# Kernel optimization log

Measured on AMD Instinct MI355X. Metric: run time of the kernel, lower is better.

Reference implementation:

```python
import jax, jax.numpy as jnp
import numpy as np

# CRPConfig defaults
KAPPA = 1.0
C = 0.95
ALPHA = 0.05
EPS = 1e-8
T_MAX = 32
MARGIN_FACTOR = 2.0

B, I, HD, L = 512, 1024, 2048, 1000


def setup_inputs() -> dict:
    key = jax.random.key(0)
    k0, k1, k2, k3 = jax.random.split(key, 4)
    x = jax.random.normal(k0, (B, I), jnp.float32)
    # kaiming-like scaling keeps activations numerically sane
    RIH = jax.random.normal(k1, (I, HD), jnp.float32) * np.float32(1.0 / np.sqrt(I))
    RH = jax.random.normal(k2, (HD, HD), jnp.float32) * np.float32(1.0 / np.sqrt(HD))
    RHL = jax.random.normal(k3, (HD, L), jnp.float32) * np.float32(1.0 / np.sqrt(HD))
    BH = jnp.zeros((HD,), jnp.float32)
    BL = jnp.zeros((L,), jnp.float32)
    MIH = jnp.ones((I, HD), jnp.float32)
    MH = jnp.ones((HD, HD), jnp.float32)
    MHL = jnp.ones((HD, L), jnp.float32)
    return {"x": x, "RIH": RIH, "RH": RH, "RHL": RHL, "BH": BH, "BL": BL,
            "MIH": MIH, "MH": MH, "MHL": MHL}


def _crp_forward(x, RIH, RH, RHL, BH, BL, MIH, MH, MHL):
    # build weights
    W_IH = RIH * MIH                      # [I, H]
    W_HL = RHL * MHL                      # [H, L]
    RHm = RH * MH                         # [H, H]
    # normalize so max column L1 <= c (value only; straight-through grad)
    col_l1 = jnp.abs(RHm).sum(axis=0)
    scale = C / jnp.maximum(col_l1.max(), EPS)
    W_H = jax.lax.stop_gradient(RHm * scale) + RHm - jax.lax.stop_gradient(RHm)

    rho = 1.0 - KAPPA + KAPPA * C
    denom = max(1e-12, 1.0 - rho)
    whl_inf = jnp.abs(W_HL).sum(axis=0).max()
    gamma_coef = whl_inf * (rho / denom)

    drive = x @ W_IH + BH                 # constant across steps, [B, H]
    Bsz = x.shape[0]
    Hs0 = jnp.zeros((Bsz, HD), x.dtype)
    active0 = jnp.ones((Bsz,), jnp.bool_)
    tau0 = jnp.full((Bsz,), T_MAX, jnp.int32)
    cert0 = jnp.zeros((Bsz,), jnp.bool_)
    logits_tau0 = jnp.zeros((Bsz, L), x.dtype)

    def step(carry, t):
        Hs, active, tau, certified, logits_tau = carry
        pre = Hs @ W_H + drive
        act = jnp.where(pre >= 0, pre, ALPHA * pre)      # LeakyReLU
        H_cand = (1.0 - KAPPA) * Hs + KAPPA * act
        H_next = jnp.where(active[:, None], H_cand, Hs)
        logits = H_next @ W_HL + BL
        # certification
        dH = jnp.max(jnp.abs(H_next - Hs), axis=1)       # H_prev == Hs
        Gamma = gamma_coef * dH
        top2 = jax.lax.top_k(logits, 2)[0]
        margin = top2[:, 0] - top2[:, 1]
        newly = active & (margin > MARGIN_FACTOR * Gamma)
        tau = jnp.where(newly, t, tau)
        certified = certified | newly
        logits_tau = jnp.where(newly[:, None], logits, logits_tau)
        active = active & (~newly)
        return (H_next, active, tau, certified, logits_tau), None

    ts = jnp.arange(1, T_MAX + 1, dtype=jnp.int32)
    (Hf, active, tau, certified, logits_tau), _ = jax.lax.scan(
        step, (Hs0, active0, tau0, cert0, logits_tau0), ts)

    never = ~certified
    logits_last = Hf @ W_HL + BL
    logits_tau = jnp.where(never[:, None], logits_last, logits_tau)
    return logits_tau


def reference(x, RIH, RH, RHL, BH, BL, MIH, MH, MHL):
    return _crp_forward(x, RIH, RH, RHL, BH, BL, MIH, MH, MHL)
```

## Files before the change

### kernel.cpp

```cpp
#include <hip/hip_runtime.h>

typedef __attribute__((ext_vector_type(8))) short short8;
typedef __attribute__((ext_vector_type(4))) float f32x4;

static constexpr int BN    = 512;
static constexpr int ID    = 1024;
static constexpr int HDm   = 2048;
static constexpr int LD    = 1000;
static constexpr int TMAXc = 32;
static constexpr float ALPHAc = 0.05f;

__device__ __forceinline__ unsigned short f2bf(float x) {
    unsigned u = __float_as_uint(x);
    u += 0x7fffu + ((u >> 16) & 1u);
    return (unsigned short)(u >> 16);
}
__device__ __forceinline__ float bf2f(unsigned short h) {
    return __uint_as_float(((unsigned)h) << 16);
}
__device__ __forceinline__ void split2(float x, unsigned short& hi, unsigned short& lo) {
    hi = f2bf(x);
    lo = f2bf(x - bf2f(hi));
}

__device__ __forceinline__ void gload16(const void* g, void* l) {
    __builtin_amdgcn_global_load_lds(
        (const __attribute__((address_space(1))) unsigned int*)g,
        (__attribute__((address_space(3))) unsigned int*)l, 16, 0, 0);
}


__device__ __forceinline__ size_t himg_off(int gr, int gc) {
    const int rt = gr >> 6, ar = gr & 63, kc = gc >> 7, ac = gc & 127;
    const int byte = (ar * 256 + ac * 2) ^ ((ar & 15) << 4);
    return ((size_t)(rt * 16 + kc) << 14) + byte;
}

__device__ __forceinline__ void tile64_drive(
    const float* __restrict__ Af, int lda, int row0,
    const unsigned short* __restrict__ BThi, const unsigned short* __restrict__ BTlo,
    int ldk, int col0, int K, char* lds, f32x4& acc, int& s_out, int& p_out)
{
    char* Ah = lds;
    char* Al = lds + 16384;
    char* Bh = lds + 32768;
    char* Bl = lds + 40960;
    const int t = threadIdx.x, lane = t & 63, w = t >> 6;
    const int s = w & 7, p = w >> 3;
    s_out = s; p_out = p;
    f32x4 z = {0.f, 0.f, 0.f, 0.f};
    acc = z;

    const int ar = t >> 4, ac = (t & 15) << 3;
    const int br = t >> 5, bc = (t & 31) << 2;
    const int asb = (ar * 256 + ac * 2) ^ ((ar & 15) << 4);
    const int bsb = (br * 256 + bc * 2) ^ ((br & 15) << 4);
    const float* Ap = Af + (size_t)(row0 + ar) * lda + ac;
    const unsigned short* Bhp = BThi + (size_t)(col0 + br) * ldk + bc;
    const unsigned short* Blp = BTlo + (size_t)(col0 + br) * ldk + bc;

    const int frow = s >> 1, fcol = s & 1;
    const int arow = frow * 16 + (lane & 15);
    const int colr = fcol * 16 + (lane & 15);
    const int ab0 = arow * 256, bb0 = colr * 256;
    const int axor = (arow & 15) << 4, bxor = (colr & 15) << 4;
    const int kwin = p * 128 + ((lane >> 4) << 4);

    float4 af0a = *(const float4*)(Ap),       af0b = *(const float4*)(Ap + 4);
    float4 af1a = *(const float4*)(Ap + 128), af1b = *(const float4*)(Ap + 132);
    uint2 bh0 = *(const uint2*)(Bhp),       bl0 = *(const uint2*)(Blp);
    uint2 bh1 = *(const uint2*)(Bhp + 128), bl1 = *(const uint2*)(Blp + 128);

    for (int k0 = 0; k0 < K; k0 += 128) {
        unsigned short h[8], l[8];
        const float vv[8] = {af0a.x, af0a.y, af0a.z, af0a.w,
                             af0b.x, af0b.y, af0b.z, af0b.w};
#pragma unroll
        for (int i = 0; i < 8; ++i) split2(vv[i], h[i], l[i]);
        uint4 awh = make_uint4((unsigned)h[0] | ((unsigned)h[1] << 16),
                               (unsigned)h[2] | ((unsigned)h[3] << 16),
                               (unsigned)h[4] | ((unsigned)h[5] << 16),
                               (unsigned)h[6] | ((unsigned)h[7] << 16));
        uint4 awl = make_uint4((unsigned)l[0] | ((unsigned)l[1] << 16),
                               (unsigned)l[2] | ((unsigned)l[3] << 16),
                               (unsigned)l[4] | ((unsigned)l[5] << 16),
                               (unsigned)l[6] | ((unsigned)l[7] << 16));
        const uint2 bwh = bh0, bwl = bl0;
        __syncthreads();
        *(uint4*)(Ah + asb) = awh;
        *(uint4*)(Al + asb) = awl;
        *(uint2*)(Bh + bsb) = bwh;
        *(uint2*)(Bl + bsb) = bwl;
        af0a = af1a; af0b = af1b;
        bh0 = bh1; bl0 = bl1;
        if (k0 + 256 < K) {
            af1a = *(const float4*)(Ap + k0 + 256);
            af1b = *(const float4*)(Ap + k0 + 260);
            bh1 = *(const uint2*)(Bhp + k0 + 256);
            bl1 = *(const uint2*)(Blp + k0 + 256);
        }
        __syncthreads();
#pragma unroll
        for (int ks = 0; ks < 2; ++ks) {
            const int kb = kwin + ks * 64;
            short8 bh = *(const short8*)(Bh + ((bb0 + kb) ^ bxor));
            short8 bl = *(const short8*)(Bl + ((bb0 + kb) ^ bxor));
            short8 ah = *(const short8*)(Ah + ((ab0 + kb) ^ axor));
            short8 al = *(const short8*)(Al + ((ab0 + kb) ^ axor));
            acc = __builtin_amdgcn_mfma_f32_16x16x32_bf16(ah, bh, acc, 0, 0, 0);
            acc = __builtin_amdgcn_mfma_f32_16x16x32_bf16(al, bh, acc, 0, 0, 0);
            acc = __builtin_amdgcn_mfma_f32_16x16x32_bf16(ah, bl, acc, 0, 0, 0);
        }
    }
}

__device__ __forceinline__ void tile64_img(
    const char* __restrict__ Ahi, const char* __restrict__ Alo,
    const char* __restrict__ Bhi, const char* __restrict__ Blo,
    char* lds, f32x4& acc, int& s_out, int& p_out)
{
    char* Ah = lds;
    char* Al = lds + 16384;
    char* Bh = lds + 32768;
    char* Bl = lds + 40960;
    const int t = threadIdx.x, lane = t & 63, w = t >> 6;
    const int s = w & 7, p = w >> 3;
    s_out = s; p_out = p;
    f32x4 z = {0.f, 0.f, 0.f, 0.f};
    acc = z;

    const int frow = s >> 1, fcol = s & 1;
    const int arow = frow * 16 + (lane & 15);
    const int colr = fcol * 16 + (lane & 15);
    const int ab0 = arow * 256, bb0 = colr * 256;
    const int axor = (arow & 15) << 4, bxor = (colr & 15) << 4;
    const int kwin = p * 128 + ((lane >> 4) << 4);
    const int t16 = t * 16;

    for (int kc = 0; kc < 16; ++kc) {
        __syncthreads();
        gload16(Ahi + ((size_t)kc << 14) + t16, Ah + (w << 10));
        gload16(Alo + ((size_t)kc << 14) + t16, Al + (w << 10));
        if (w < 8) gload16(Bhi + ((size_t)kc << 13) + t16, Bh + (w << 10));
        else       gload16(Blo + ((size_t)kc << 13) + t16 - 8192, Bl + ((w - 8) << 10));
        __syncthreads();
#pragma unroll
        for (int ks = 0; ks < 2; ++ks) {
            const int kb = kwin + ks * 64;
            short8 bh = *(const short8*)(Bh + ((bb0 + kb) ^ bxor));
            short8 bl = *(const short8*)(Bl + ((bb0 + kb) ^ bxor));
            short8 ah = *(const short8*)(Ah + ((ab0 + kb) ^ axor));
            short8 al = *(const short8*)(Al + ((ab0 + kb) ^ axor));
            acc = __builtin_amdgcn_mfma_f32_16x16x32_bf16(ah, bh, acc, 0, 0, 0);
            acc = __builtin_amdgcn_mfma_f32_16x16x32_bf16(al, bh, acc, 0, 0, 0);
            acc = __builtin_amdgcn_mfma_f32_16x16x32_bf16(ah, bl, acc, 0, 0, 0);
        }
    }
}

__device__ __forceinline__ void tile32_img(
    const char* __restrict__ Ahi, const char* __restrict__ Alo,
    const char* __restrict__ Bhi, const char* __restrict__ Blo,
    char* lds, f32x4& acc, int& s_out, int& p_out)
{
    char* Ah = lds;
    char* Al = lds + 8192;
    char* Bh = lds + 16384;
    char* Bl = lds + 24576;
    const int t = threadIdx.x, lane = t & 63, w = t >> 6;
    const int s = w & 3, p = w >> 2;
    s_out = s; p_out = p;
    f32x4 z = {0.f, 0.f, 0.f, 0.f};
    acc = z;

    const int frow = s >> 1, fcol = s & 1;
    const int arow = frow * 16 + (lane & 15);
    const int colr = fcol * 16 + (lane & 15);
    const int ab0 = arow * 256, bb0 = colr * 256;
    const int axor = (arow & 15) << 4, bxor = (colr & 15) << 4;
    const int kwin = p * 64 + ((lane >> 4) << 4);
    const int t16 = t * 16;

    for (int kc = 0; kc < 16; ++kc) {
        __syncthreads();
        if (w < 8) {
            gload16(Ahi + ((size_t)kc << 14) + t16, Ah + (w << 10));
            gload16(Bhi + ((size_t)kc << 13) + t16, Bh + (w << 10));
        } else {
            gload16(Alo + ((size_t)kc << 14) + t16 - 8192, Al + ((w - 8) << 10));
            gload16(Blo + ((size_t)kc << 13) + t16 - 8192, Bl + ((w - 8) << 10));
        }
        __syncthreads();
        const int kb = kwin;
        short8 bh = *(const short8*)(Bh + ((bb0 + kb) ^ bxor));
        short8 bl = *(const short8*)(Bl + ((bb0 + kb) ^ bxor));
        short8 ah = *(const short8*)(Ah + ((ab0 + kb) ^ axor));
        short8 al = *(const short8*)(Al + ((ab0 + kb) ^ axor));
        acc = __builtin_amdgcn_mfma_f32_16x16x32_bf16(ah, bh, acc, 0, 0, 0);
        acc = __builtin_amdgcn_mfma_f32_16x16x32_bf16(al, bh, acc, 0, 0, 0);
        acc = __builtin_amdgcn_mfma_f32_16x16x32_bf16(ah, bl, acc, 0, 0, 0);
    }
}

__global__ void k_init(int* active, int* cnt, float* scal,
                       float* margS, float* drift, int* fresh)
{
    int i = blockIdx.x * blockDim.x + threadIdx.x;
    if (i < 2 * BN) {
        active[i] = 1;
        margS[i] = 3.4e38f;
        drift[i] = 0.f;
        fresh[i] = 1;
    }
    if (i < 16) cnt[i] = 64;
    if (i < 8) scal[i] = 0.f;
}

__global__ __launch_bounds__(256) void k_colsum_wh(const float* __restrict__ RH,
                                                   const float* __restrict__ MH,
                                                   float* __restrict__ part)
{
    const int colTile = blockIdx.x >> 3, rs = blockIdx.x & 7;
    const int col = colTile * 64 + (threadIdx.x & 63);
    const int rq = threadIdx.x >> 6;
    const int r0 = rs * 256;
    float s = 0.f;
    for (int i = r0 + rq; i < r0 + 256; i += 4)
        s += fabsf(RH[(size_t)i * HDm + col] * MH[(size_t)i * HDm + col]);
    __shared__ float red[4][64];
    red[rq][threadIdx.x & 63] = s;
    __syncthreads();
    if (threadIdx.x < 64)
        part[(size_t)rs * HDm + col] = red[0][threadIdx.x] + red[1][threadIdx.x] +
                                       red[2][threadIdx.x] + red[3][threadIdx.x];
}

__global__ __launch_bounds__(256) void k_colsum_whl(const float* __restrict__ RHL,
                                                    const float* __restrict__ MHL,
                                                    float* __restrict__ part)
{
    const int colTile = blockIdx.x >> 3, rs = blockIdx.x & 7;
    const int col = colTile * 64 + (threadIdx.x & 63);
    const int rq = threadIdx.x >> 6;
    const int r0 = rs * 256;
    float s = 0.f;
    if (col < LD) {
        for (int i = r0 + rq; i < r0 + 256; i += 4)
            s += fabsf(RHL[(size_t)i * LD + col] * MHL[(size_t)i * LD + col]);
    }
    __shared__ float red[4][64];
    red[rq][threadIdx.x & 63] = s;
    __syncthreads();
    if (threadIdx.x < 64)
        part[(size_t)rs * 1024 + col] = red[0][threadIdx.x] + red[1][threadIdx.x] +
                                        red[2][threadIdx.x] + red[3][threadIdx.x];
}

__global__ __launch_bounds__(1024) void k_scalars(const float* __restrict__ part_wh,
                                                  const float* __restrict__ part_whl,
                                                  float* scal)
{
    float m1 = 0.f, m2 = 0.f;
    for (int c = threadIdx.x; c < HDm; c += 1024) {
        float s = 0.f;
#pragma unroll
        for (int k = 0; k < 8; ++k) s += part_wh[(size_t)k * HDm + c];
        m1 = fmaxf(m1, s);
    }
    {
        const int c = threadIdx.x;
        if (c < 1024) {
            float s = 0.f;
#pragma unroll
            for (int k = 0; k < 8; ++k) s += part_whl[(size_t)k * 1024 + c];
            m2 = fmaxf(m2, s);
        }
    }
#pragma unroll
    for (int off = 1; off < 64; off <<= 1) {
        m1 = fmaxf(m1, __shfl_xor(m1, off));
        m2 = fmaxf(m2, __shfl_xor(m2, off));
    }
    __shared__ float r1[16], r2[16];
    if ((threadIdx.x & 63) == 0) { r1[threadIdx.x >> 6] = m1; r2[threadIdx.x >> 6] = m2; }
    __syncthreads();
    if (threadIdx.x == 0) {
        float a = 0.f, b = 0.f;
#pragma unroll
        for (int i = 0; i < 16; ++i) { a = fmaxf(a, r1[i]); b = fmaxf(b, r2[i]); }
        scal[2] = 0.95f / fmaxf(a, 1e-8f);
        scal[3] = b * 19.f;
    }
}

__global__ __launch_bounds__(256) void k_wsplit(
    const float* __restrict__ R, const float* __restrict__ M,
    unsigned short* __restrict__ Ohi, unsigned short* __restrict__ Olo,
    int NR, int NC, int NCp, const float* __restrict__ scal, int scidx)
{
    __shared__ float T[64][65];
    const int nct = NCp >> 6;
    const int c0 = (blockIdx.x % nct) << 6;
    const int r0 = (blockIdx.x / nct) << 6;
    const float s = (scidx >= 0) ? scal[scidx] : 1.f;
    const int t = threadIdx.x;
    const int ir = t >> 2, ics = (t & 3) << 4;
#pragma unroll
    for (int i = 0; i < 16; ++i) {
        const int c = c0 + ics + i;
        float v = 0.f;
        if (c < NC) {
            const size_t idx = (size_t)(r0 + ir) * NC + c;
            v = R[idx] * M[idx] * s;
        }
        T[ir][ics + i] = v;
    }
    __syncthreads();
    const int oc = t >> 2, ors = (t & 3) << 4;
    unsigned short hb[16], lb[16];
#pragma unroll
    for (int i = 0; i < 16; ++i) split2(T[ors + i][oc], hb[i], lb[i]);
    const size_t base = (size_t)(c0 + oc) * NR + r0 + ors;
    uint4 v;
    v.x = hb[0] | ((unsigned)hb[1] << 16);  v.y = hb[2] | ((unsigned)hb[3] << 16);
    v.z = hb[4] | ((unsigned)hb[5] << 16);  v.w = hb[6] | ((unsigned)hb[7] << 16);
    *(uint4*)(Ohi + base) = v;
    v.x = hb[8] | ((unsigned)hb[9] << 16);  v.y = hb[10] | ((unsigned)hb[11] << 16);
    v.z = hb[12] | ((unsigned)hb[13] << 16); v.w = hb[14] | ((unsigned)hb[15] << 16);
    *(uint4*)(Ohi + base + 8) = v;
    v.x = lb[0] | ((unsigned)lb[1] << 16);  v.y = lb[2] | ((unsigned)lb[3] << 16);
    v.z = lb[4] | ((unsigned)lb[5] << 16);  v.w = lb[6] | ((unsigned)lb[7] << 16);
    *(uint4*)(Olo + base) = v;
    v.x = lb[8] | ((unsigned)lb[9] << 16);  v.y = lb[10] | ((unsigned)lb[11] << 16);
    v.z = lb[12] | ((unsigned)lb[13] << 16); v.w = lb[14] | ((unsigned)lb[15] << 16);
    *(uint4*)(Olo + base + 8) = v;
}

__global__ __launch_bounds__(256) void k_wsplit_img(
    const float* __restrict__ R, const float* __restrict__ M,
    char* __restrict__ imghi, char* __restrict__ imglo,
    int NC, int nkc, const float* __restrict__ scal, int scidx)
{
    const int ct = blockIdx.x / nkc, kc = blockIdx.x % nkc;
    const float s = (scidx >= 0) ? scal[scidx] : 1.f;
    char* hi = imghi + ((size_t)(ct * nkc + kc) << 13);
    char* lo = imglo + ((size_t)(ct * nkc + kc) << 13);
#pragma unroll
    for (int i = 0; i < 16; ++i) {
        const int idx = i * 256 + threadIdx.x;
        const int br = idx & 31, bc = idx >> 5;
        const int c = ct * 32 + br;
        const int k = kc * 128 + bc;
        float v = 0.f;
        if (c < NC) { const size_t a = (size_t)k * NC + c; v = R[a] * M[a] * s; }
        unsigned short h, l;
        split2(v, h, l);
        const int byte = (br * 256 + bc * 2) ^ ((br & 15) << 4);
        *(unsigned short*)(hi + byte) = h;
        *(unsigned short*)(lo + byte) = l;
    }
}

__global__ __launch_bounds__(1024, 8) void k_drive_mfma(
    const float* __restrict__ x,
    const unsigned short* __restrict__ WIHThi, const unsigned short* __restrict__ WIHTlo,
    const float* __restrict__ BH, float* __restrict__ drive)
{
    __shared__ char lds[49152];
    f32x4 acc;
    int s, p;
    const int row0 = (blockIdx.x >> 6) * 64, col0 = (blockIdx.x & 63) * 32;
    tile64_drive(x, ID, row0, WIHThi, WIHTlo, ID, col0, ID, lds, acc, s, p);
    const int lane = threadIdx.x & 63;
    __syncthreads();
    f32x4* red = (f32x4*)lds;
    if (p == 1) red[s * 64 + lane] = acc;
    __syncthreads();
    if (p == 0) {
        f32x4 o = red[s * 64 + lane];
        acc += o;
        const int frow = s >> 1, fcol = s & 1;
        const int gc = col0 + fcol * 16 + (lane & 15);
        const int gr0 = row0 + frow * 16 + ((lane >> 4) << 2);
        const float bh = BH[gc];
#pragma unroll
        for (int r = 0; r < 4; ++r)
            drive[(size_t)(gr0 + r) * HDm + gc] = acc[r] + bh;
    }
}

__global__ __launch_bounds__(1024, 8) void k_p1(
    const char* __restrict__ WHhi, const char* __restrict__ WHlo,
    const float* __restrict__ drive,
    char* __restrict__ HAhi, char* __restrict__ HAlo,
    char* __restrict__ HBhi, char* __restrict__ HBlo,
    const float* __restrict__ logits, float* __restrict__ out,
    int* __restrict__ active, int* __restrict__ cnt, const float* __restrict__ scal,
    float* __restrict__ dhp, const float* __restrict__ m1p, const float* __restrict__ m2p,
    float* __restrict__ margS, float* __restrict__ drift, const int* __restrict__ fresh,
    int t)
{
    __shared__ char lds[49152];
    __shared__ int sact[64], snew[64];
    __shared__ int s_cnt;
    const int pp = (t - 1) & 1, pc = t & 1;
    {
        const int* cp = cnt + pp * 8;
        int sum = 0;
#pragma unroll
        for (int i = 0; i < 8; ++i) sum += cp[i];
        if (sum == 0) return;
    }
    const int bid = blockIdx.x, tid = threadIdx.x;
    const int rt = bid >> 6, row0m = rt << 6, col0 = (bid & 63) * 32;
    const int* actP = active + pp * BN;
    int* actC = active + pc * BN;
    const char* Hshi = (t & 1) ? HAhi : HBhi;
    const char* Hslo = (t & 1) ? HAlo : HBlo;
    char* Hnhi = (t & 1) ? HBhi : HAhi;
    char* Hnlo = (t & 1) ? HBlo : HAlo;
    const float* dhpP = dhp + (size_t)pp * BN * 64;
    float* dhpC = dhp + (size_t)pc * BN * 64;
    const float* margSP = margS + pp * BN;
    float* margSC = margS + pc * BN;
    const float* driftP = drift + pp * BN;
    float* driftC = drift + pc * BN;
    const int* freshP = fresh + pp * BN;

    if (t > 1) {
        const float gamma2 = 2.f * scal[3];
        const int rl = tid >> 4, j = tid & 15;
        const int r = row0m + rl;
        const int act = actP[r];
        const int fr = freshP[r];
        float dh = fmaxf(fmaxf(dhpP[(size_t)r * 64 + j],      dhpP[(size_t)r * 64 + 16 + j]),
                         fmaxf(dhpP[(size_t)r * 64 + 32 + j], dhpP[(size_t)r * 64 + 48 + j]));
        float M1 = m1p[(size_t)r * 32 + j], M2 = m2p[(size_t)r * 32 + j];
        {
            float o1 = m1p[(size_t)r * 32 + 16 + j], o2 = m2p[(size_t)r * 32 + 16 + j];
            if (o1 > M1) { M2 = fmaxf(M1, o2); M1 = o1; }
            else M2 = fmaxf(M2, o1);
        }
#pragma unroll
        for (int off = 1; off < 16; off <<= 1) {
            dh = fmaxf(dh, __shfl_xor(dh, off));
            float o1 = __shfl_xor(M1, off), o2 = __shfl_xor(M2, off);
            if (o1 > M1) { M2 = fmaxf(M1, o2); M1 = o1; }
            else M2 = fmaxf(M2, o1);
        }
        if (j == 0) {
            const float marg = M1 - M2;
            int nw = fr && act && (marg > gamma2 * dh);
            snew[rl] = nw;
            sact[rl] = act && !nw;
            margSC[r] = fr ? marg : margSP[r];
            driftC[r] = fr ? 0.f : (driftP[r] + dh);
        }
    } else if (tid < 64) {
        sact[tid] = 1; snew[tid] = 0;
    }
    __syncthreads();
    if (tid < 64) {
        unsigned long long b = __ballot(sact[tid] != 0);
        actC[row0m + tid] = sact[tid];
        if (tid == 0) {
            s_cnt = __popcll(b);
            (cnt + pc * 8)[rt] = s_cnt;
        }
    }
    if (t > 1 && (bid & 63) == 0) {
        for (int rl2 = 0; rl2 < 64; ++rl2) {
            if (snew[rl2]) {
                const float* lr = logits + (size_t)(row0m + rl2) * LD;
                float* orow = out + (size_t)(row0m + rl2) * LD;
                for (int jj = tid; jj < LD; jj += 1024) orow[jj] = lr[jj];
            }
        }
    }
    __syncthreads();
    if (s_cnt == 0) return;

    f32x4 acc;
    int s, p;
    tile64_img(Hshi + ((size_t)(rt * 16) << 14), Hslo + ((size_t)(rt * 16) << 14),
               WHhi + ((size_t)((bid & 63) * 16) << 13), WHlo + ((size_t)((bid & 63) * 16) << 13),
               lds, acc, s, p);
    const int lane = tid & 63;
    __syncthreads();
    f32x4* red = (f32x4*)lds;
    if (p == 1) red[s * 64 + lane] = acc;
    __syncthreads();
    float (*sdh)[2] = (float(*)[2])(lds + 16384);
    if (p == 0) {
        f32x4 o = red[s * 64 + lane];
        acc += o;
        const int frow = s >> 1, fcol = s & 1;
        const int gc = col0 + fcol * 16 + (lane & 15);
        const int gr0 = row0m + frow * 16 + ((lane >> 4) << 2);
        float dh4[4];
#pragma unroll
        for (int r = 0; r < 4; ++r) {
            const int gr = gr0 + r;
            const size_t ia = himg_off(gr, gc);
            const unsigned short oh = *(const unsigned short*)(Hshi + ia);
            const unsigned short ol = *(const unsigned short*)(Hslo + ia);
            const float old = bf2f(oh) + bf2f(ol);
            const int a = sact[gr - row0m];
            unsigned short nh, nl;
            if (a) {
                const float pre = acc[r] + drive[(size_t)gr * HDm + gc];
                const float av = pre >= 0.f ? pre : ALPHAc * pre;
                split2(av, nh, nl);
            } else { nh = oh; nl = ol; }
            *(unsigned short*)(Hnhi + ia) = nh;
            *(unsigned short*)(Hnlo + ia) = nl;
            dh4[r] = fabsf((bf2f(nh) + bf2f(nl)) - old);
        }
#pragma unroll
        for (int off = 1; off < 16; off <<= 1)
#pragma unroll
            for (int r = 0; r < 4; ++r)
                dh4[r] = fmaxf(dh4[r], __shfl_xor(dh4[r], off));
        if ((lane & 15) == 0) {
            const int rl0 = frow * 16 + ((lane >> 4) << 2);
#pragma unroll
            for (int r = 0; r < 4; ++r) sdh[rl0 + r][fcol] = dh4[r];
        }
    }
    __syncthreads();
    if (tid < 64) {
        float d = fmaxf(sdh[tid][0], sdh[tid][1]);
        dhpC[(size_t)(row0m + tid) * 64 + (bid & 63)] = d;
    }
}

__global__ __launch_bounds__(1024, 8) void k_p2(
    const char* __restrict__ WLhi, const char* __restrict__ WLlo,
    const float* __restrict__ BL,
    const char* __restrict__ HAhi, const char* __restrict__ HAlo,
    const char* __restrict__ HBhi, const char* __restrict__ HBlo,
    float* __restrict__ logits, const int* __restrict__ active, const int* __restrict__ cnt,
    float* __restrict__ m1p, float* __restrict__ m2p, const float* __restrict__ scal,
    const float* __restrict__ dhp, const float* __restrict__ margS,
    const float* __restrict__ drift, int* __restrict__ fresh, int t)
{
    __shared__ char lds[33280];
    __shared__ int sposs[32];
    __shared__ int s_go;
    const int pc = t & 1;
    {
        const int* cp = cnt + pc * 8;
        int sum = 0;
#pragma unroll
        for (int i = 0; i < 8; ++i) sum += cp[i];
        if (sum == 0) return;
    }
    const int bid = blockIdx.x, tid = threadIdx.x;
    const char* Hnhi = (t & 1) ? HBhi : HAhi;
    const char* Hnlo = (t & 1) ? HBlo : HAlo;
    const int* actC = active + pc * BN;
    const float* dhpC = dhp + (size_t)pc * BN * 64;
    const float* margSc = margS + pc * BN;
    const float* driftc = drift + pc * BN;
    int* freshC = fresh + pc * BN;
    const int row0 = (bid >> 5) * 32, col0 = (bid & 31) * 32;

    {
        const int rr = tid >> 5, j = tid & 31;
        const int r = row0 + rr;
        float d = fmaxf(dhpC[(size_t)r * 64 + j], dhpC[(size_t)r * 64 + 32 + j]);
#pragma unroll
        for (int off = 1; off < 32; off <<= 1) d = fmaxf(d, __shfl_xor(d, off));
        if (j == 0) {
            const int act = actC[r];
            int poss;
            if (t == TMAXc) poss = act;
            else {
                const float whl = scal[3] * (1.f / 19.f);
                poss = act && (margSc[r] + 2.f * whl * (driftc[r] + d) >
                               0.99f * 38.f * whl * d);
            }
            sposs[rr] = poss;
        }
    }
    __syncthreads();
    if (tid < 64) {
        int v = (tid < 32) ? sposs[tid] : 0;
        unsigned long long b = __ballot(v != 0);
        if (tid == 0) s_go = (b != 0ull);
    }
    __syncthreads();
    if (tid < 32) freshC[row0 + tid] = s_go;
    if (!s_go) return;

    const int rt2 = bid >> 5;
    const char* Ahi = Hnhi + ((size_t)((rt2 >> 1) * 16) << 14) + ((rt2 & 1) << 13);
    const char* Alo = Hnlo + ((size_t)((rt2 >> 1) * 16) << 14) + ((rt2 & 1) << 13);
    f32x4 acc;
    int s, p;
    tile32_img(Ahi, Alo,
               WLhi + ((size_t)((bid & 31) * 16) << 13), WLlo + ((size_t)((bid & 31) * 16) << 13),
               lds, acc, s, p);
    const int lane = tid & 63;
    __syncthreads();
    f32x4* red = (f32x4*)lds;
    if (p > 0) red[(p - 1) * 256 + s * 64 + lane] = acc;
    __syncthreads();
    float (*st1)[2] = (float(*)[2])(lds + 12288);
    float (*st2)[2] = (float(*)[2])(lds + 12544);
    if (p == 0) {
#pragma unroll
        for (int q = 0; q < 3; ++q) {
            f32x4 o = red[q * 256 + s * 64 + lane];
            acc += o;
        }
        const int frow = s >> 1, fcol = s & 1;
        const int gc = col0 + fcol * 16 + (lane & 15);
        const int gr0 = row0 + frow * 16 + ((lane >> 4) << 2);
        const bool okc = gc < LD;
        const float blv = okc ? BL[gc] : 0.f;
        float m1a[4], m2a[4];
#pragma unroll
        for (int r = 0; r < 4; ++r) {
            const float v = acc[r] + blv;
            if (okc) logits[(size_t)(gr0 + r) * LD + gc] = v;
            m1a[r] = okc ? v : -3.4e38f;
            m2a[r] = -3.4e38f;
        }
#pragma unroll
        for (int off = 1; off < 16; off <<= 1) {
#pragma unroll
            for (int r = 0; r < 4; ++r) {
                float o1 = __shfl_xor(m1a[r], off);
                float o2 = __shfl_xor(m2a[r], off);
                if (o1 > m1a[r]) { m2a[r] = fmaxf(m1a[r], o2); m1a[r] = o1; }
                else m2a[r] = fmaxf(m2a[r], o1);
            }
        }
        if ((lane & 15) == 0) {
            const int rl0 = frow * 16 + ((lane >> 4) << 2);
#pragma unroll
            for (int r = 0; r < 4; ++r) {
                st1[rl0 + r][fcol] = m1a[r];
                st2[rl0 + r][fcol] = m2a[r];
            }
        }
    }
    __syncthreads();
    if (tid < 32) {
        float M1 = st1[tid][0], M2 = st2[tid][0];
        {
            float o1 = st1[tid][1], o2 = st2[tid][1];
            if (o1 > M1) { M2 = fmaxf(M1, o2); M1 = o1; }
            else M2 = fmaxf(M2, o1);
        }
        m1p[(size_t)(row0 + tid) * 32 + (bid & 31)] = M1;
        m2p[(size_t)(row0 + tid) * 32 + (bid & 31)] = M2;
    }
}

__global__ __launch_bounds__(1024) void k_tail(
    const float* __restrict__ logits, const int* __restrict__ active,
    float* __restrict__ out)
{
    const int row0 = blockIdx.x * 64;
    for (int rl = 0; rl < 64; ++rl) {
        const int r = row0 + rl;
        if (active[r] && active[BN + r]) {
            const float* lr = logits + (size_t)r * LD;
            float* orow = out + (size_t)r * LD;
            for (int jj = threadIdx.x; jj < LD; jj += 1024) orow[jj] = lr[jj];
        }
    }
}

extern "C" void kernel_launch(void* const* d_in, const int* in_sizes, int n_in,
                              void* d_out, int out_size, void* d_ws, size_t ws_size,
                              hipStream_t stream)
{
    const float* x   = (const float*)d_in[0];
    const float* RIH = (const float*)d_in[1];
    const float* RH  = (const float*)d_in[2];
    const float* RHL = (const float*)d_in[3];
    const float* BH  = (const float*)d_in[4];
    const float* BL  = (const float*)d_in[5];
    const float* MIH = (const float*)d_in[6];
    const float* MH  = (const float*)d_in[7];
    const float* MHL = (const float*)d_in[8];
    float* out = (float*)d_out;
    char* w = (char*)d_ws;

    char* WHhi = w;
    char* WHlo = w + 8388608;
    char* WXhi = w + 16777216;
    char* WXlo = w + 20971520;
    float* drive = (float*)(w + 25165824);
    char* HAhi = w + 29360128;
    char* HAlo = w + 31457280;
    char* HBhi = w + 33554432;
    char* HBlo = w + 35651584;
    float* logits = (float*)(w + 37748736);
    float* scal   = (float*)(w + 39796736);
    int*   active = (int*)(w + 39796800);
    int*   cnt    = (int*)(w + 39800896);
    float* dhp    = (float*)(w + 39800960);
    float* m1p    = (float*)(w + 40063104);
    float* m2p    = (float*)(w + 40128640);
    float* margS  = (float*)(w + 40194176);
    float* drift  = (float*)(w + 40198272);
    int*   fresh  = (int*)(w + 40202368);

    k_init<<<4, 256, 0, stream>>>(active, cnt, scal, margS, drift, fresh);
    k_colsum_wh<<<256, 256, 0, stream>>>(RH, MH, dhp);
    k_colsum_whl<<<128, 256, 0, stream>>>(RHL, MHL, m1p);
    k_scalars<<<1, 1024, 0, stream>>>(dhp, m1p, scal);
    k_wsplit<<<512, 256, 0, stream>>>(RIH, MIH, (unsigned short*)WXhi,
                                      (unsigned short*)WXlo, ID, HDm, HDm, scal, -1);
    k_drive_mfma<<<512, 1024, 0, stream>>>(x, (const unsigned short*)WXhi,
                                           (const unsigned short*)WXlo, BH, drive);
    k_wsplit_img<<<1024, 256, 0, stream>>>(RH, MH, WHhi, WHlo, HDm, 16, scal, 2);
    k_wsplit_img<<<512, 256, 0, stream>>>(RHL, MHL, WXhi, WXlo, LD, 16, scal, -1);
    (void)hipMemsetAsync(HAhi, 0, 4194304, stream);

    for (int t = 1; t <= TMAXc; ++t) {
        k_p1<<<512, 1024, 0, stream>>>(WHhi, WHlo, drive, HAhi, HAlo, HBhi, HBlo,
                                       logits, out, active, cnt, scal, dhp, m1p, m2p,
                                       margS, drift, fresh, t);
        k_p2<<<512, 1024, 0, stream>>>(WXhi, WXlo, BL, HAhi, HAlo, HBhi, HBlo,
                                       logits, active, cnt, m1p, m2p, scal,
                                       dhp, margS, drift, fresh, t);
    }
    k_tail<<<8, 1024, 0, stream>>>(logits, active, out);
}
```

Before: 1.336 ms.

## Double-buffer LDS tiles with 64-wide K chunks in recurrent GEMM kernels

Re-lays out the pre-swizzled weight and hidden-state images into 64-column K chunks instead of 128, and rewrites the per-step tile loops to double-buffer LDS so the next chunk's global-to-LDS load is issued while MFMAs consume the current one. This replaces two block barriers per chunk with a single wait-plus-barrier. The aim is to hide global load latency in the 32-step scan. In the logits kernel, only half the waves now compute and the K-split reduction shrinks from four partial sums to two. The cost is twice as many loop iterations with smaller work per barrier, and idle waves in the second kernel.

New measurement: 1.767 ms. 1.32x slower.

```diff
diff --git a/kernel.cpp b/kernel.cpp
--- a/kernel.cpp
+++ b/kernel.cpp
@@ -31,9 +31,9 @@
 
 
 __device__ __forceinline__ size_t himg_off(int gr, int gc) {
-    const int rt = gr >> 6, ar = gr & 63, kc = gc >> 7, ac = gc & 127;
-    const int byte = (ar * 256 + ac * 2) ^ ((ar & 15) << 4);
-    return ((size_t)(rt * 16 + kc) << 14) + byte;
+    const int rt = gr >> 6, ar = gr & 63, kc = gc >> 6, ac = gc & 63;
+    const int byte = (ar * 128 + ac * 2) ^ ((ar & 15) << 4);
+    return ((size_t)(rt * 32 + kc) << 13) + byte;
 }
 
 __device__ __forceinline__ void tile64_drive(
@@ -114,92 +114,118 @@
     }
 }
 
-__device__ __forceinline__ void tile64_img(
+__device__ __forceinline__ void tile64_pipe(
     const char* __restrict__ Ahi, const char* __restrict__ Alo,
     const char* __restrict__ Bhi, const char* __restrict__ Blo,
     char* lds, f32x4& acc, int& s_out, int& p_out)
 {
-    char* Ah = lds;
-    char* Al = lds + 16384;
-    char* Bh = lds + 32768;
-    char* Bl = lds + 40960;
     const int t = threadIdx.x, lane = t & 63, w = t >> 6;
     const int s = w & 7, p = w >> 3;
     s_out = s; p_out = p;
     f32x4 z = {0.f, 0.f, 0.f, 0.f};
     acc = z;
-
     const int frow = s >> 1, fcol = s & 1;
     const int arow = frow * 16 + (lane & 15);
     const int colr = fcol * 16 + (lane & 15);
-    const int ab0 = arow * 256, bb0 = colr * 256;
     const int axor = (arow & 15) << 4, bxor = (colr & 15) << 4;
-    const int kwin = p * 128 + ((lane >> 4) << 4);
-    const int t16 = t * 16;
-
-    for (int kc = 0; kc < 16; ++kc) {
-        __syncthreads();
-        gload16(Ahi + ((size_t)kc << 14) + t16, Ah + (w << 10));
-        gload16(Alo + ((size_t)kc << 14) + t16, Al + (w << 10));
-        if (w < 8) gload16(Bhi + ((size_t)kc << 13) + t16, Bh + (w << 10));
-        else       gload16(Blo + ((size_t)kc << 13) + t16 - 8192, Bl + ((w - 8) << 10));
-        __syncthreads();
-#pragma unroll
-        for (int ks = 0; ks < 2; ++ks) {
-            const int kb = kwin + ks * 64;
-            short8 bh = *(const short8*)(Bh + ((bb0 + kb) ^ bxor));
-            short8 bl = *(const short8*)(Bl + ((bb0 + kb) ^ bxor));
-            short8 ah = *(const short8*)(Ah + ((ab0 + kb) ^ axor));
-            short8 al = *(const short8*)(Al + ((ab0 + kb) ^ axor));
-            acc = __builtin_amdgcn_mfma_f32_16x16x32_bf16(ah, bh, acc, 0, 0, 0);
-            acc = __builtin_amdgcn_mfma_f32_16x16x32_bf16(al, bh, acc, 0, 0, 0);
-            acc = __builtin_amdgcn_mfma_f32_16x16x32_bf16(ah, bl, acc, 0, 0, 0);
-        }
-    }
-}
-
-__device__ __forceinline__ void tile32_img(
+    const int kwin = p * 64 + ((lane >> 4) << 4);
+    const int abyte = (arow * 128 + kwin) ^ axor;
+    const int bbyte = (colr * 128 + kwin) ^ bxor;
+    const int l16 = lane << 4;
+
+    char* buf0 = lds;
+    char* buf1 = lds + 24576;
+
+#define P1_ISSUE(kc, buf)                                                      \
+    do {                                                                       \
+        if (w < 8) {                                                           \
+            gload16(Ahi + ((size_t)(kc) << 13) + (w << 10) + l16,              \
+                    (buf) + (w << 10));                                        \
+            if (w < 4)                                                         \
+                gload16(Bhi + ((size_t)(kc) << 12) + (w << 10) + l16,          \
+                        (buf) + 16384 + (w << 10));                            \
+            else                                                               \
+                gload16(Blo + ((size_t)(kc) << 12) + ((w - 4) << 10) + l16,    \
+                        (buf) + 20480 + ((w - 4) << 10));                      \
+        } else {                                                               \
+            gload16(Alo + ((size_t)(kc) << 13) + ((w - 8) << 10) + l16,        \
+                    (buf) + 8192 + ((w - 8) << 10));                           \
+        }                                                                      \
+    } while (0)
+
+    P1_ISSUE(0, buf0);
+    for (int kc = 0; kc < 32; ++kc) {
+        char* cur = (kc & 1) ? buf1 : buf0;
+        char* nxt = (kc & 1) ? buf0 : buf1;
+        asm volatile("s_waitcnt vmcnt(0)" ::: "memory");
+        __builtin_amdgcn_sched_barrier(0);
+        __builtin_amdgcn_s_barrier();
+        __builtin_amdgcn_sched_barrier(0);
+        if (kc + 1 < 32) P1_ISSUE(kc + 1, nxt);
+        short8 ah = *(const short8*)(cur + abyte);
+        short8 al = *(const short8*)(cur + 8192 + abyte);
+        short8 bh = *(const short8*)(cur + 16384 + bbyte);
+        short8 bl = *(const short8*)(cur + 20480 + bbyte);
+        acc = __builtin_amdgcn_mfma_f32_16x16x32_bf16(ah, bh, acc, 0, 0, 0);
+        acc = __builtin_amdgcn_mfma_f32_16x16x32_bf16(al, bh, acc, 0, 0, 0);
+        acc = __builtin_amdgcn_mfma_f32_16x16x32_bf16(ah, bl, acc, 0, 0, 0);
+    }
+#undef P1_ISSUE
+}
+
+__device__ __forceinline__ void tile32_pipe(
     const char* __restrict__ Ahi, const char* __restrict__ Alo,
     const char* __restrict__ Bhi, const char* __restrict__ Blo,
     char* lds, f32x4& acc, int& s_out, int& p_out)
 {
-    char* Ah = lds;
-    char* Al = lds + 8192;
-    char* Bh = lds + 16384;
-    char* Bl = lds + 24576;
     const int t = threadIdx.x, lane = t & 63, w = t >> 6;
     const int s = w & 3, p = w >> 2;
     s_out = s; p_out = p;
     f32x4 z = {0.f, 0.f, 0.f, 0.f};
     acc = z;
-
     const int frow = s >> 1, fcol = s & 1;
     const int arow = frow * 16 + (lane & 15);
     const int colr = fcol * 16 + (lane & 15);
-    const int ab0 = arow * 256, bb0 = colr * 256;
     const int axor = (arow & 15) << 4, bxor = (colr & 15) << 4;
-    const int kwin = p * 64 + ((lane >> 4) << 4);
-    const int t16 = t * 16;
-
-    for (int kc = 0; kc < 16; ++kc) {
-        __syncthreads();
-        if (w < 8) {
-            gload16(Ahi + ((size_t)kc << 14) + t16, Ah + (w << 10));
-            gload16(Bhi + ((size_t)kc << 13) + t16, Bh + (w << 10));
-        } else {
-            gload16(Alo + ((size_t)kc << 14) + t16 - 8192, Al + ((w - 8) << 10));
-            gload16(Blo + ((size_t)kc << 13) + t16 - 8192, Bl + ((w - 8) << 10));
-        }
-        __syncthreads();
-        const int kb = kwin;
-        short8 bh = *(const short8*)(Bh + ((bb0 + kb) ^ bxor));
-        short8 bl = *(const short8*)(Bl + ((bb0 + kb) ^ bxor));
-        short8 ah = *(const short8*)(Ah + ((ab0 + kb) ^ axor));
-        short8 al = *(const short8*)(Al + ((ab0 + kb) ^ axor));
-        acc = __builtin_amdgcn_mfma_f32_16x16x32_bf16(ah, bh, acc, 0, 0, 0);
-        acc = __builtin_amdgcn_mfma_f32_16x16x32_bf16(al, bh, acc, 0, 0, 0);
-        acc = __builtin_amdgcn_mfma_f32_16x16x32_bf16(ah, bl, acc, 0, 0, 0);
-    }
+    const int kwin = (p & 1) * 64 + ((lane >> 4) << 4);
+    const int abyte = (arow * 128 + kwin) ^ axor;
+    const int bbyte = (colr * 128 + kwin) ^ bxor;
+    const int g = w & 3;
+    const int l16 = lane << 4;
+
+    char* buf0 = lds;
+    char* buf1 = lds + 16384;
+
+#define P2_ISSUE(kc, buf)                                                      \
+    do {                                                                       \
+        const char* src;                                                       \
+        if (w < 4)       src = Ahi + ((size_t)(kc) << 13) + (g << 10);         \
+        else if (w < 8)  src = Alo + ((size_t)(kc) << 13) + (g << 10);         \
+        else if (w < 12) src = Bhi + ((size_t)(kc) << 12) + (g << 10);         \
+        else             src = Blo + ((size_t)(kc) << 12) + (g << 10);         \
+        gload16(src + l16, (buf) + (w << 10));                                 \
+    } while (0)
+
+    P2_ISSUE(0, buf0);
+    for (int kc = 0; kc < 32; ++kc) {
+        char* cur = (kc & 1) ? buf1 : buf0;
+        char* nxt = (kc & 1) ? buf0 : buf1;
+        asm volatile("s_waitcnt vmcnt(0)" ::: "memory");
+        __builtin_amdgcn_sched_barrier(0);
+        __builtin_amdgcn_s_barrier();
+        __builtin_amdgcn_sched_barrier(0);
+        if (kc + 1 < 32) P2_ISSUE(kc + 1, nxt);
+        if (p < 2) {
+            short8 ah = *(const short8*)(cur + abyte);
+            short8 al = *(const short8*)(cur + 4096 + abyte);
+            short8 bh = *(const short8*)(cur + 8192 + bbyte);
+            short8 bl = *(const short8*)(cur + 12288 + bbyte);
+            acc = __builtin_amdgcn_mfma_f32_16x16x32_bf16(ah, bh, acc, 0, 0, 0);
+            acc = __builtin_amdgcn_mfma_f32_16x16x32_bf16(al, bh, acc, 0, 0, 0);
+            acc = __builtin_amdgcn_mfma_f32_16x16x32_bf16(ah, bl, acc, 0, 0, 0);
+        }
+    }
+#undef P2_ISSUE
 }
 
 __global__ void k_init(int* active, int* cnt, float* scal,
@@ -339,25 +365,24 @@
 __global__ __launch_bounds__(256) void k_wsplit_img(
     const float* __restrict__ R, const float* __restrict__ M,
     char* __restrict__ imghi, char* __restrict__ imglo,
-    int NC, int nkc, const float* __restrict__ scal, int scidx)
-{
-    const int ct = blockIdx.x / nkc, kc = blockIdx.x % nkc;
+    int NC, const float* __restrict__ scal, int scidx)
+{
+    const int ct = blockIdx.x >> 5, kc = blockIdx.x & 31;
     const float s = (scidx >= 0) ? scal[scidx] : 1.f;
-    char* hi = imghi + ((size_t)(ct * nkc + kc) << 13);
-    char* lo = imglo + ((size_t)(ct * nkc + kc) << 13);
-#pragma unroll
-    for (int i = 0; i < 16; ++i) {
+    const size_t base = (size_t)blockIdx.x << 12;
+#pragma unroll
+    for (int i = 0; i < 8; ++i) {
         const int idx = i * 256 + threadIdx.x;
         const int br = idx & 31, bc = idx >> 5;
         const int c = ct * 32 + br;
-        const int k = kc * 128 + bc;
+        const int k = kc * 64 + bc;
         float v = 0.f;
         if (c < NC) { const size_t a = (size_t)k * NC + c; v = R[a] * M[a] * s; }
         unsigned short h, l;
         split2(v, h, l);
-        const int byte = (br * 256 + bc * 2) ^ ((br & 15) << 4);
-        *(unsigned short*)(hi + byte) = h;
-        *(unsigned short*)(lo + byte) = l;
+        const int byte = (br * 128 + bc * 2) ^ ((br & 15) << 4);
+        *(unsigned short*)(imghi + base + byte) = h;
+        *(unsigned short*)(imglo + base + byte) = l;
     }
 }
 
@@ -482,9 +507,9 @@
 
     f32x4 acc;
     int s, p;
-    tile64_img(Hshi + ((size_t)(rt * 16) << 14), Hslo + ((size_t)(rt * 16) << 14),
-               WHhi + ((size_t)((bid & 63) * 16) << 13), WHlo + ((size_t)((bid & 63) * 16) << 13),
-               lds, acc, s, p);
+    tile64_pipe(Hshi + ((size_t)(rt * 32) << 13), Hslo + ((size_t)(rt * 32) << 13),
+                WHhi + ((size_t)((bid & 63) * 32) << 12), WHlo + ((size_t)((bid & 63) * 32) << 12),
+                lds, acc, s, p);
     const int lane = tid & 63;
     __syncthreads();
     f32x4* red = (f32x4*)lds;
@@ -594,26 +619,23 @@
     if (!s_go) return;
 
     const int rt2 = bid >> 5;
-    const char* Ahi = Hnhi + ((size_t)((rt2 >> 1) * 16) << 14) + ((rt2 & 1) << 13);
-    const char* Alo = Hnlo + ((size_t)((rt2 >> 1) * 16) << 14) + ((rt2 & 1) << 13);
+    const char* Ahi = Hnhi + ((size_t)((rt2 >> 1) * 32) << 13) + ((rt2 & 1) << 12);
+    const char* Alo = Hnlo + ((size_t)((rt2 >> 1) * 32) << 13) + ((rt2 & 1) << 12);
     f32x4 acc;
     int s, p;
-    tile32_img(Ahi, Alo,
-               WLhi + ((size_t)((bid & 31) * 16) << 13), WLlo + ((size_t)((bid & 31) * 16) << 13),
-               lds, acc, s, p);
+    tile32_pipe(Ahi, Alo,
+                WLhi + ((size_t)((bid & 31) * 32) << 12), WLlo + ((size_t)((bid & 31) * 32) << 12),
+                lds, acc, s, p);
     const int lane = tid & 63;
     __syncthreads();
     f32x4* red = (f32x4*)lds;
-    if (p > 0) red[(p - 1) * 256 + s * 64 + lane] = acc;
-    __syncthreads();
-    float (*st1)[2] = (float(*)[2])(lds + 12288);
-    float (*st2)[2] = (float(*)[2])(lds + 12544);
+    if (p == 1) red[s * 64 + lane] = acc;
+    __syncthreads();
+    float (*st1)[2] = (float(*)[2])(lds + 8192);
+    float (*st2)[2] = (float(*)[2])(lds + 8448);
     if (p == 0) {
-#pragma unroll
-        for (int q = 0; q < 3; ++q) {
-            f32x4 o = red[q * 256 + s * 64 + lane];
-            acc += o;
-        }
+        f32x4 o = red[s * 64 + lane];
+        acc += o;
         const int frow = s >> 1, fcol = s & 1;
         const int gc = col0 + fcol * 16 + (lane & 15);
         const int gr0 = row0 + frow * 16 + ((lane >> 4) << 2);
@@ -718,8 +740,8 @@
                                       (unsigned short*)WXlo, ID, HDm, HDm, scal, -1);
     k_drive_mfma<<<512, 1024, 0, stream>>>(x, (const unsigned short*)WXhi,
                                            (const unsigned short*)WXlo, BH, drive);
-    k_wsplit_img<<<1024, 256, 0, stream>>>(RH, MH, WHhi, WHlo, HDm, 16, scal, 2);
-    k_wsplit_img<<<512, 256, 0, stream>>>(RHL, MHL, WXhi, WXlo, LD, 16, scal, -1);
+    k_wsplit_img<<<2048, 256, 0, stream>>>(RH, MH, WHhi, WHlo, HDm, scal, 2);
+    k_wsplit_img<<<1024, 256, 0, stream>>>(RHL, MHL, WXhi, WXlo, LD, scal, -1);
     (void)hipMemsetAsync(HAhi, 0, 4194304, stream);
 
     for (int t = 1; t <= TMAXc; ++t) {
```
